# Kernel tuning notes

Measured on AMD Instinct MI355X. Metric: run time of the kernel, lower is better.

The kernel has to match this reference:

```python
import jax, jax.numpy as jnp
import numpy as np

N_NODES = 100000


def _gcn_layer(x, src, dst, W, b, n_nodes):
    # x: [N, Cin]; src/dst already include self-loops
    h = x @ W  # [N, Cout]
    deg = jax.ops.segment_sum(jnp.ones_like(dst, dtype=h.dtype), dst,
                              num_segments=n_nodes)  # in-degree incl. self-loop
    dinv = jnp.where(deg > 0, deg ** -0.5, 0.0)
    norm = dinv[src] * dinv[dst]  # [E]
    msg = h[src] * norm[:, None]  # [E, Cout]
    out = jax.ops.segment_sum(msg, dst, num_segments=n_nodes)
    return out + b


def setup_inputs() -> dict:
    key = jax.random.key(0)
    k1, k2, k3, k4, k5, k6, k7 = jax.random.split(key, 7)
    E = 6400000
    x = jax.random.normal(k1, (N_NODES, 5), dtype=jnp.float32)
    edge_index = jax.random.randint(k2, (2, E), 0, N_NODES, dtype=jnp.int64)
    edge_f = jax.random.normal(k3, (E,), dtype=jnp.float32)
    edge_attr = jax.random.normal(k4, (E, 1), dtype=jnp.float32)
    # GCNConv params (glorot-ish scale)
    W1 = jax.random.normal(k5, (5, 8), dtype=jnp.float32) * (1.0 / np.sqrt(5))
    b1 = jnp.zeros((8,), dtype=jnp.float32)
    W2 = jax.random.normal(k6, (8, 5), dtype=jnp.float32) * (1.0 / np.sqrt(8))
    b2 = jnp.zeros((5,), dtype=jnp.float32)
    return {"x": x, "edge_index": edge_index, "edge_f": edge_f,
            "edge_attr": edge_attr, "W1": W1, "b1": b1, "W2": W2, "b2": b2}


def reference(x, edge_index, edge_f, edge_attr, W1, b1, W2, b2):
    n = x.shape[0]
    loops = jnp.arange(n, dtype=edge_index.dtype)
    src = jnp.concatenate([edge_index[0], loops])  # add self-loops (PyG default)
    dst = jnp.concatenate([edge_index[1], loops])
    h = _gcn_layer(x, src, dst, W1, b1, n)
    h = _gcn_layer(h, src, dst, W2, b2, n)
    return h
```

## Files before the change

kernel.cpp:

```cpp
#include <hip/hip_runtime.h>
#include <hip/hip_fp16.h>


#define TPB 256
#define VPB 256
#define B_BITS 8
#define MAXB 512
#define CAP 17408
#define NBLK_E 512
#define EPB 12500
#define SCT 512
#define DGT 512

typedef int int4e __attribute__((ext_vector_type(4)));
typedef _Float16 h8 __attribute__((ext_vector_type(8)));

__device__ __forceinline__ int4e ld4(const int* p) {
    return *(const int4e*)p;
}

__global__ void k_init(int B, int* __restrict__ bpos) {
    int b = blockIdx.x * blockDim.x + threadIdx.x;
    if (b < B) bpos[b] = b * CAP;
}

__global__ __launch_bounds__(SCT) void k_scat(const int* __restrict__ src,
        const int* __restrict__ dst, int E, int B,
        int* __restrict__ bpos, int* __restrict__ pairs) {
    __shared__ int sorted[EPB];
    __shared__ int hist[MAXB], scn[MAXB], cur[MAXB], gbase[MAXB];
    int t = threadIdx.x;
    for (int i = t; i < MAXB; i += SCT) hist[i] = 0;
    __syncthreads();
    int lo = blockIdx.x * EPB;
    int n = min(E - lo, EPB);
    int n4 = n & ~3;
    for (int i = t * 4; i < n4; i += SCT * 4) {
        int4e d4 = ld4(dst + lo + i);
        atomicAdd(&hist[d4.x >> B_BITS], 1);
        atomicAdd(&hist[d4.y >> B_BITS], 1);
        atomicAdd(&hist[d4.z >> B_BITS], 1);
        atomicAdd(&hist[d4.w >> B_BITS], 1);
    }
    for (int i = n4 + t; i < n; i += SCT)
        atomicAdd(&hist[dst[lo + i] >> B_BITS], 1);
    __syncthreads();
    if (t < MAXB) scn[t] = hist[t];
    __syncthreads();
    for (int off = 1; off < MAXB; off <<= 1) {
        int v = (t >= off && t < MAXB) ? scn[t - off] : 0;
        __syncthreads();
        if (t < MAXB) scn[t] += v;
        __syncthreads();
    }
    if (t < MAXB) {
        int h = hist[t];
        cur[t] = scn[t] - h;
        gbase[t] = (t < B && h) ? atomicAdd(&bpos[t], h) : 0;
    }
    __syncthreads();
    for (int i = t * 4; i < n4; i += SCT * 4) {
        int4e d4 = ld4(dst + lo + i);
        int4e s4 = ld4(src + lo + i);
        int p;
        p = atomicAdd(&cur[d4.x >> B_BITS], 1); sorted[p] = (s4.x << B_BITS) | (d4.x & (VPB - 1));
        p = atomicAdd(&cur[d4.y >> B_BITS], 1); sorted[p] = (s4.y << B_BITS) | (d4.y & (VPB - 1));
        p = atomicAdd(&cur[d4.z >> B_BITS], 1); sorted[p] = (s4.z << B_BITS) | (d4.z & (VPB - 1));
        p = atomicAdd(&cur[d4.w >> B_BITS], 1); sorted[p] = (s4.w << B_BITS) | (d4.w & (VPB - 1));
    }
    for (int i = n4 + t; i < n; i += SCT) {
        int d = dst[lo + i], s = src[lo + i];
        int p = atomicAdd(&cur[d >> B_BITS], 1);
        sorted[p] = (s << B_BITS) | (d & (VPB - 1));
    }
    __syncthreads();
    int wave = t >> 6, lane = t & 63;
    for (int bb = wave; bb < B; bb += (SCT >> 6)) {
        int h = hist[bb];
        int st = scn[bb] - h;
        int gb = gbase[bb];
        for (int j = lane; j < h; j += 64)
            pairs[gb + j] = sorted[st + j];
    }
}

__global__ __launch_bounds__(DGT) void k_pre(const int* __restrict__ pairs,
        const int* __restrict__ bpos, const float* __restrict__ x,
        unsigned int* __restrict__ jinfo, _Float16* __restrict__ xs, int N) {
    __shared__ int hist[VPB];
    __shared__ int scn[VPB];
    int t = threadIdx.x, b = blockIdx.x;
    if (t < VPB) hist[t] = 0;
    __syncthreads();
    int base = b * CAP;
    int n = bpos[b] - base, n4 = n & ~3;
    for (int i = t * 4; i < n4; i += DGT * 4) {
        int4e p = ld4(pairs + base + i);
        atomicAdd(&hist[p.x & (VPB - 1)], 1);
        atomicAdd(&hist[p.y & (VPB - 1)], 1);
        atomicAdd(&hist[p.z & (VPB - 1)], 1);
        atomicAdd(&hist[p.w & (VPB - 1)], 1);
    }
    for (int i = n4 + t; i < n; i += DGT)
        atomicAdd(&hist[pairs[base + i] & (VPB - 1)], 1);
    __syncthreads();
    if (t < VPB) scn[t] = hist[t];
    __syncthreads();
    for (int off = 1; off < VPB; off <<= 1) {
        int v = (t >= off && t < VPB) ? scn[t - off] : 0;
        __syncthreads();
        if (t < VPB) scn[t] += v;
        __syncthreads();
    }
    int node = b * VPB + t;
    if (t < VPB && node < N) {
        int h = hist[t];
        int start = base + scn[t] - h;
        jinfo[node] = ((unsigned int)start << 9) | (unsigned int)h;
        float di = rsqrtf((float)(h + 1));
        const float* xp = x + (size_t)node * 5;
        h8 v;
        v[0] = (_Float16)(xp[0] * di); v[1] = (_Float16)(xp[1] * di);
        v[2] = (_Float16)(xp[2] * di); v[3] = (_Float16)(xp[3] * di);
        v[4] = (_Float16)(xp[4] * di);
        v[5] = (_Float16)0.f; v[6] = (_Float16)0.f; v[7] = (_Float16)0.f;
        *(h8*)(xs + (size_t)node * 8) = v;
    }
}

__global__ __launch_bounds__(1024) void k_ag1(int* __restrict__ pairs,
        const int* __restrict__ bpos, const unsigned int* __restrict__ jinfo,
        const _Float16* __restrict__ xs, const float* __restrict__ b1,
        const float* __restrict__ W1, const float* __restrict__ W2,
        _Float16* __restrict__ h2s, int N) {
    __shared__ int csr[CAP];
    __shared__ int js[VPB], ct[VPB], cur[VPB];
    int t = threadIdx.x, b = blockIdx.x;
    int base = b * CAP;
    if (t < VPB) {
        int node = b * VPB + t;
        int s = 0, c = 0;
        if (node < N) {
            unsigned int u = jinfo[node];
            s = (int)(u >> 9) - base;
            c = (int)(u & 511u);
        }
        js[t] = s; ct[t] = c; cur[t] = s;
    }
    __syncthreads();
    int n = bpos[b] - base, n4 = n & ~3;
    for (int i = t * 4; i < n4; i += 1024 * 4) {
        int4e p = ld4(pairs + base + i);
        int q;
        q = atomicAdd(&cur[p.x & (VPB - 1)], 1); csr[q] = p.x >> B_BITS;
        q = atomicAdd(&cur[p.y & (VPB - 1)], 1); csr[q] = p.y >> B_BITS;
        q = atomicAdd(&cur[p.z & (VPB - 1)], 1); csr[q] = p.z >> B_BITS;
        q = atomicAdd(&cur[p.w & (VPB - 1)], 1); csr[q] = p.w >> B_BITS;
    }
    for (int i = n4 + t; i < n; i += 1024) {
        int p = pairs[base + i];
        int q = atomicAdd(&cur[p & (VPB - 1)], 1);
        csr[q] = p >> B_BITS;
    }
    __syncthreads();
    for (int i = t; i < n; i += 1024)
        pairs[base + i] = csr[i];
    int lane = t & 3, ln = t >> 2;
    int node = b * VPB + ln;
    if (node >= N) return;
    int s0 = js[ln], cn = ct[ln];
    float a0 = 0.f, a1 = 0.f, a2 = 0.f, a3 = 0.f, a4 = 0.f;
    int j = lane;
    for (; j + 12 < cn; j += 16) {
        int sA = csr[s0 + j];
        int sB = csr[s0 + j + 4];
        int sC = csr[s0 + j + 8];
        int sD = csr[s0 + j + 12];
        h8 vA = *(const h8*)(xs + (size_t)sA * 8);
        h8 vB = *(const h8*)(xs + (size_t)sB * 8);
        h8 vC = *(const h8*)(xs + (size_t)sC * 8);
        h8 vD = *(const h8*)(xs + (size_t)sD * 8);
        a0 += (float)vA[0] + (float)vB[0] + (float)vC[0] + (float)vD[0];
        a1 += (float)vA[1] + (float)vB[1] + (float)vC[1] + (float)vD[1];
        a2 += (float)vA[2] + (float)vB[2] + (float)vC[2] + (float)vD[2];
        a3 += (float)vA[3] + (float)vB[3] + (float)vC[3] + (float)vD[3];
        a4 += (float)vA[4] + (float)vB[4] + (float)vC[4] + (float)vD[4];
    }
    for (; j < cn; j += 4) {
        int sA = csr[s0 + j];
        h8 vA = *(const h8*)(xs + (size_t)sA * 8);
        a0 += (float)vA[0]; a1 += (float)vA[1]; a2 += (float)vA[2];
        a3 += (float)vA[3]; a4 += (float)vA[4];
    }
#pragma unroll
    for (int d = 1; d < 4; d <<= 1) {
        a0 += __shfl_xor(a0, d); a1 += __shfl_xor(a1, d);
        a2 += __shfl_xor(a2, d); a3 += __shfl_xor(a3, d);
        a4 += __shfl_xor(a4, d);
    }
    h8 sv = *(const h8*)(xs + (size_t)node * 8);
    float tc[5];
    tc[0] = a0 + (float)sv[0]; tc[1] = a1 + (float)sv[1];
    tc[2] = a2 + (float)sv[2]; tc[3] = a3 + (float)sv[3];
    tc[4] = a4 + (float)sv[4];
    float di = rsqrtf((float)(cn + 1));
    float o1[8];
#pragma unroll
    for (int jj = 0; jj < 8; ++jj) {
        float h = 0.f;
#pragma unroll
        for (int c = 0; c < 5; ++c) h += tc[c] * W1[c * 8 + jj];
        o1[jj] = h * di + b1[jj];
    }
    if (lane == 0) {
        float hv[5];
#pragma unroll
        for (int k = 0; k < 5; ++k) {
            float h = 0.f;
#pragma unroll
            for (int jj = 0; jj < 8; ++jj) h += o1[jj] * W2[jj * 5 + k];
            hv[k] = h * di;
        }
        h8 w;
        w[0] = (_Float16)hv[0]; w[1] = (_Float16)hv[1]; w[2] = (_Float16)hv[2];
        w[3] = (_Float16)hv[3]; w[4] = (_Float16)hv[4];
        w[5] = (_Float16)0.f; w[6] = (_Float16)0.f; w[7] = (_Float16)0.f;
        *(h8*)(h2s + (size_t)node * 8) = w;
    }
}

__device__ __forceinline__ void g_map(int g, int t, int* node, int* lane) {
    int q = g >> 6, r = g & 63;
    int b = q * 8 + (r & 7);
    int s = r >> 3;
    *node = b * VPB + s * 32 + (t >> 3);
    *lane = t & 7;
}

__global__ __launch_bounds__(TPB) void k_g2(const int* __restrict__ pairs,
        const unsigned int* __restrict__ jinfo, const _Float16* __restrict__ h2s,
        const float* __restrict__ b2, float* __restrict__ out, int N) {
    int node, lane;
    g_map(blockIdx.x, threadIdx.x, &node, &lane);
    if (node >= N) return;
    unsigned int u = jinfo[node];
    int jsa = (int)(u >> 9), cn = (int)(u & 511u);
    float a0 = 0.f, a1 = 0.f, a2 = 0.f, a3 = 0.f, a4 = 0.f;
    int j = lane;
    if (j + 24 < cn) {
        int iA = pairs[jsa + j],      iB = pairs[jsa + j + 8];
        int iC = pairs[jsa + j + 16], iD = pairs[jsa + j + 24];
        for (;;) {
            int nj = j + 32;
            bool more = (nj + 24 < cn);
            int pA, pB, pC, pD;
            if (more) {
                pA = pairs[jsa + nj];      pB = pairs[jsa + nj + 8];
                pC = pairs[jsa + nj + 16]; pD = pairs[jsa + nj + 24];
            }
            h8 vA = *(const h8*)(h2s + (size_t)iA * 8);
            h8 vB = *(const h8*)(h2s + (size_t)iB * 8);
            h8 vC = *(const h8*)(h2s + (size_t)iC * 8);
            h8 vD = *(const h8*)(h2s + (size_t)iD * 8);
            a0 += (float)vA[0] + (float)vB[0] + (float)vC[0] + (float)vD[0];
            a1 += (float)vA[1] + (float)vB[1] + (float)vC[1] + (float)vD[1];
            a2 += (float)vA[2] + (float)vB[2] + (float)vC[2] + (float)vD[2];
            a3 += (float)vA[3] + (float)vB[3] + (float)vC[3] + (float)vD[3];
            a4 += (float)vA[4] + (float)vB[4] + (float)vC[4] + (float)vD[4];
            if (!more) break;
            iA = pA; iB = pB; iC = pC; iD = pD; j = nj;
        }
        j += 32;
    }
    for (; j < cn; j += 8) {
        int sA = pairs[jsa + j];
        h8 vA = *(const h8*)(h2s + (size_t)sA * 8);
        a0 += (float)vA[0]; a1 += (float)vA[1]; a2 += (float)vA[2];
        a3 += (float)vA[3]; a4 += (float)vA[4];
    }
#pragma unroll
    for (int d = 1; d < 8; d <<= 1) {
        a0 += __shfl_xor(a0, d); a1 += __shfl_xor(a1, d);
        a2 += __shfl_xor(a2, d); a3 += __shfl_xor(a3, d);
        a4 += __shfl_xor(a4, d);
    }
    if (lane == 0) {
        float di = rsqrtf((float)(cn + 1));
        h8 sv = *(const h8*)(h2s + (size_t)node * 8);
        float* op = out + (size_t)node * 5;
        op[0] = (a0 + (float)sv[0]) * di + b2[0];
        op[1] = (a1 + (float)sv[1]) * di + b2[1];
        op[2] = (a2 + (float)sv[2]) * di + b2[2];
        op[3] = (a3 + (float)sv[3]) * di + b2[3];
        op[4] = (a4 + (float)sv[4]) * di + b2[4];
    }
}

extern "C" void kernel_launch(void* const* d_in, const int* in_sizes, int n_in,
                              void* d_out, int out_size, void* d_ws, size_t ws_size,
                              hipStream_t stream) {
    const float* x   = (const float*)d_in[0];
    const int*  eidx = (const int*)d_in[1];
    const float* W1 = (const float*)d_in[4];
    const float* b1 = (const float*)d_in[5];
    const float* W2 = (const float*)d_in[6];
    const float* b2 = (const float*)d_in[7];
    float* out = (float*)d_out;

    const int N = in_sizes[0] / 5;
    const int E = in_sizes[1] / 2;
    const int* src = eidx;
    const int* dst = eidx + E;

    const int B = (N + VPB - 1) / VPB;

    int*      pairs = (int*)d_ws;
    _Float16* xs    = (_Float16*)(pairs + (size_t)B * CAP);
    _Float16* h2s   = xs + (size_t)8 * N;
    unsigned int* jinfo = (unsigned int*)(h2s + (size_t)8 * N);
    int*      bpos  = (int*)(jinfo + N);

    const int gG = ((B + 7) / 8) * 64;

    k_init <<<(B + TPB - 1) / TPB, TPB, 0, stream>>>(B, bpos);
    k_scat <<<NBLK_E, SCT, 0, stream>>>(src, dst, E, B, bpos, pairs);
    k_pre  <<<B, DGT, 0, stream>>>(pairs, bpos, x, jinfo, xs, N);
    k_ag1  <<<B, 1024, 0, stream>>>(pairs, bpos, jinfo, xs, b1, W1, W2, h2s, N);
    k_g2   <<<gG, TPB, 0, stream>>>(pairs, jinfo, h2s, b2, out, N);
}
```

Before: 225.1 us.

## Retune scatter grid, deepen ag1 gather unroll, defer CSR writeback, narrow g2 lanes

The scatter kernel's grid size is now derived from E with a smaller edges-per-block value, where before it was a fixed block count. In the first aggregation kernel, the gather gets an 8-wide unrolled loop to keep more loads in flight, and the CSR writeback to global memory moves after the compute so it no longer delays the gathers. The second gather kernel uses 4 lanes per node instead of 8, so each block covers twice as many nodes and the grid has half as many blocks. The aim is more memory-level parallelism and less idle lane work on nodes with small degree, at the cost of more register pressure and different load balance.

```diff
diff --git a/kernel.cpp b/kernel.cpp
--- a/kernel.cpp
+++ b/kernel.cpp
@@ -7,8 +7,7 @@
 #define B_BITS 8
 #define MAXB 512
 #define CAP 17408
-#define NBLK_E 512
-#define EPB 12500
+#define EPB 11200
 #define SCT 512
 #define DGT 512
 
@@ -163,19 +162,38 @@
         csr[q] = p >> B_BITS;
     }
     __syncthreads();
-    for (int i = t; i < n; i += 1024)
-        pairs[base + i] = csr[i];
     int lane = t & 3, ln = t >> 2;
     int node = b * VPB + ln;
-    if (node >= N) return;
     int s0 = js[ln], cn = ct[ln];
     float a0 = 0.f, a1 = 0.f, a2 = 0.f, a3 = 0.f, a4 = 0.f;
     int j = lane;
+    for (; j + 28 < cn; j += 32) {
+        int sA = csr[s0 + j];      int sB = csr[s0 + j + 4];
+        int sC = csr[s0 + j + 8];  int sD = csr[s0 + j + 12];
+        int sE = csr[s0 + j + 16]; int sF = csr[s0 + j + 20];
+        int sG = csr[s0 + j + 24]; int sH = csr[s0 + j + 28];
+        h8 vA = *(const h8*)(xs + (size_t)sA * 8);
+        h8 vB = *(const h8*)(xs + (size_t)sB * 8);
+        h8 vC = *(const h8*)(xs + (size_t)sC * 8);
+        h8 vD = *(const h8*)(xs + (size_t)sD * 8);
+        h8 vE = *(const h8*)(xs + (size_t)sE * 8);
+        h8 vF = *(const h8*)(xs + (size_t)sF * 8);
+        h8 vG = *(const h8*)(xs + (size_t)sG * 8);
+        h8 vH = *(const h8*)(xs + (size_t)sH * 8);
+        a0 += ((float)vA[0] + (float)vB[0]) + ((float)vC[0] + (float)vD[0])
+            + ((float)vE[0] + (float)vF[0]) + ((float)vG[0] + (float)vH[0]);
+        a1 += ((float)vA[1] + (float)vB[1]) + ((float)vC[1] + (float)vD[1])
+            + ((float)vE[1] + (float)vF[1]) + ((float)vG[1] + (float)vH[1]);
+        a2 += ((float)vA[2] + (float)vB[2]) + ((float)vC[2] + (float)vD[2])
+            + ((float)vE[2] + (float)vF[2]) + ((float)vG[2] + (float)vH[2]);
+        a3 += ((float)vA[3] + (float)vB[3]) + ((float)vC[3] + (float)vD[3])
+            + ((float)vE[3] + (float)vF[3]) + ((float)vG[3] + (float)vH[3]);
+        a4 += ((float)vA[4] + (float)vB[4]) + ((float)vC[4] + (float)vD[4])
+            + ((float)vE[4] + (float)vF[4]) + ((float)vG[4] + (float)vH[4]);
+    }
     for (; j + 12 < cn; j += 16) {
-        int sA = csr[s0 + j];
-        int sB = csr[s0 + j + 4];
-        int sC = csr[s0 + j + 8];
-        int sD = csr[s0 + j + 12];
+        int sA = csr[s0 + j];      int sB = csr[s0 + j + 4];
+        int sC = csr[s0 + j + 8];  int sD = csr[s0 + j + 12];
         h8 vA = *(const h8*)(xs + (size_t)sA * 8);
         h8 vB = *(const h8*)(xs + (size_t)sB * 8);
         h8 vC = *(const h8*)(xs + (size_t)sC * 8);
@@ -198,43 +216,47 @@
         a2 += __shfl_xor(a2, d); a3 += __shfl_xor(a3, d);
         a4 += __shfl_xor(a4, d);
     }
-    h8 sv = *(const h8*)(xs + (size_t)node * 8);
-    float tc[5];
-    tc[0] = a0 + (float)sv[0]; tc[1] = a1 + (float)sv[1];
-    tc[2] = a2 + (float)sv[2]; tc[3] = a3 + (float)sv[3];
-    tc[4] = a4 + (float)sv[4];
-    float di = rsqrtf((float)(cn + 1));
-    float o1[8];
-#pragma unroll
-    for (int jj = 0; jj < 8; ++jj) {
-        float h = 0.f;
-#pragma unroll
-        for (int c = 0; c < 5; ++c) h += tc[c] * W1[c * 8 + jj];
-        o1[jj] = h * di + b1[jj];
-    }
-    if (lane == 0) {
-        float hv[5];
-#pragma unroll
-        for (int k = 0; k < 5; ++k) {
+    if (node < N) {
+        h8 sv = *(const h8*)(xs + (size_t)node * 8);
+        float tc[5];
+        tc[0] = a0 + (float)sv[0]; tc[1] = a1 + (float)sv[1];
+        tc[2] = a2 + (float)sv[2]; tc[3] = a3 + (float)sv[3];
+        tc[4] = a4 + (float)sv[4];
+        float di = rsqrtf((float)(cn + 1));
+        float o1[8];
+#pragma unroll
+        for (int jj = 0; jj < 8; ++jj) {
             float h = 0.f;
 #pragma unroll
-            for (int jj = 0; jj < 8; ++jj) h += o1[jj] * W2[jj * 5 + k];
-            hv[k] = h * di;
+            for (int c = 0; c < 5; ++c) h += tc[c] * W1[c * 8 + jj];
+            o1[jj] = h * di + b1[jj];
         }
-        h8 w;
-        w[0] = (_Float16)hv[0]; w[1] = (_Float16)hv[1]; w[2] = (_Float16)hv[2];
-        w[3] = (_Float16)hv[3]; w[4] = (_Float16)hv[4];
-        w[5] = (_Float16)0.f; w[6] = (_Float16)0.f; w[7] = (_Float16)0.f;
-        *(h8*)(h2s + (size_t)node * 8) = w;
-    }
+        if (lane == 0) {
+            float hv[5];
+#pragma unroll
+            for (int k = 0; k < 5; ++k) {
+                float h = 0.f;
+#pragma unroll
+                for (int jj = 0; jj < 8; ++jj) h += o1[jj] * W2[jj * 5 + k];
+                hv[k] = h * di;
+            }
+            h8 w;
+            w[0] = (_Float16)hv[0]; w[1] = (_Float16)hv[1]; w[2] = (_Float16)hv[2];
+            w[3] = (_Float16)hv[3]; w[4] = (_Float16)hv[4];
+            w[5] = (_Float16)0.f; w[6] = (_Float16)0.f; w[7] = (_Float16)0.f;
+            *(h8*)(h2s + (size_t)node * 8) = w;
+        }
+    }
+    for (int i = t; i < n; i += 1024)
+        pairs[base + i] = csr[i];
 }
 
 __device__ __forceinline__ void g_map(int g, int t, int* node, int* lane) {
-    int q = g >> 6, r = g & 63;
+    int q = g >> 5, r = g & 31;
     int b = q * 8 + (r & 7);
     int s = r >> 3;
-    *node = b * VPB + s * 32 + (t >> 3);
-    *lane = t & 7;
+    *node = b * VPB + s * 64 + (t >> 2);
+    *lane = t & 3;
 }
 
 __global__ __launch_bounds__(TPB) void k_g2(const int* __restrict__ pairs,
@@ -247,16 +269,16 @@
     int jsa = (int)(u >> 9), cn = (int)(u & 511u);
     float a0 = 0.f, a1 = 0.f, a2 = 0.f, a3 = 0.f, a4 = 0.f;
     int j = lane;
-    if (j + 24 < cn) {
-        int iA = pairs[jsa + j],      iB = pairs[jsa + j + 8];
-        int iC = pairs[jsa + j + 16], iD = pairs[jsa + j + 24];
+    if (j + 12 < cn) {
+        int iA = pairs[jsa + j],     iB = pairs[jsa + j + 4];
+        int iC = pairs[jsa + j + 8], iD = pairs[jsa + j + 12];
         for (;;) {
-            int nj = j + 32;
-            bool more = (nj + 24 < cn);
+            int nj = j + 16;
+            bool more = (nj + 12 < cn);
             int pA, pB, pC, pD;
             if (more) {
-                pA = pairs[jsa + nj];      pB = pairs[jsa + nj + 8];
-                pC = pairs[jsa + nj + 16]; pD = pairs[jsa + nj + 24];
+                pA = pairs[jsa + nj];     pB = pairs[jsa + nj + 4];
+                pC = pairs[jsa + nj + 8]; pD = pairs[jsa + nj + 12];
             }
             h8 vA = *(const h8*)(h2s + (size_t)iA * 8);
             h8 vB = *(const h8*)(h2s + (size_t)iB * 8);
@@ -270,16 +292,16 @@
             if (!more) break;
             iA = pA; iB = pB; iC = pC; iD = pD; j = nj;
         }
-        j += 32;
-    }
-    for (; j < cn; j += 8) {
+        j += 16;
+    }
+    for (; j < cn; j += 4) {
         int sA = pairs[jsa + j];
         h8 vA = *(const h8*)(h2s + (size_t)sA * 8);
         a0 += (float)vA[0]; a1 += (float)vA[1]; a2 += (float)vA[2];
         a3 += (float)vA[3]; a4 += (float)vA[4];
     }
 #pragma unroll
-    for (int d = 1; d < 8; d <<= 1) {
+    for (int d = 1; d < 4; d <<= 1) {
         a0 += __shfl_xor(a0, d); a1 += __shfl_xor(a1, d);
         a2 += __shfl_xor(a2, d); a3 += __shfl_xor(a3, d);
         a4 += __shfl_xor(a4, d);
@@ -313,6 +335,7 @@
     const int* dst = eidx + E;
 
     const int B = (N + VPB - 1) / VPB;
+    const int NBLK_E = (E + EPB - 1) / EPB;
 
     int*      pairs = (int*)d_ws;
     _Float16* xs    = (_Float16*)(pairs + (size_t)B * CAP);
@@ -320,7 +343,7 @@
     unsigned int* jinfo = (unsigned int*)(h2s + (size_t)8 * N);
     int*      bpos  = (int*)(jinfo + N);
 
-    const int gG = ((B + 7) / 8) * 64;
+    const int gG = ((B + 7) / 8) * 32;
 
     k_init <<<(B + TPB - 1) / TPB, TPB, 0, stream>>>(B, bpos);
     k_scat <<<NBLK_E, SCT, 0, stream>>>(src, dst, E, B, bpos, pairs);
```

After: 231.0 us. 1.03x slower.
